# Optimization experiments

Measured on AMD Instinct MI355X. Metric: run time of the kernel, lower is better.

## Reference

```python
import jax, jax.numpy as jnp
import numpy as np

N_NODES = 100000
N_EDGES = 3200000
NFEAT = 256
NCLASS = 64


def setup_inputs() -> dict:
    key = jax.random.key(0)
    k1, k2, k3 = jax.random.split(key, 3)
    x = jax.random.normal(k1, (N_NODES, NFEAT), dtype=jnp.float32)
    W = jax.random.normal(k2, (NFEAT, NCLASS), dtype=jnp.float32) * (1.0 / np.sqrt(NFEAT))
    b = jnp.zeros((NCLASS,), dtype=jnp.float32)
    edge_index = jax.random.randint(k3, (2, N_EDGES), 0, N_NODES, dtype=jnp.int64)
    return {"x": x, "W": W, "b": b, "edge_index": edge_index}


def reference(x, W, b, edge_index):
    # GCNConv (PyG defaults): add self-loops, symmetric D^-1/2 A D^-1/2 norm,
    # linear transform, bias.
    n = x.shape[0]
    loops = jnp.arange(n, dtype=edge_index.dtype)
    src = jnp.concatenate([edge_index[0], loops])  # [E+N]
    dst = jnp.concatenate([edge_index[1], loops])
    ew = jnp.ones(src.shape[0], dtype=x.dtype)
    deg = jax.ops.segment_sum(ew, dst, num_segments=n)  # in-degree incl. self-loop
    dinv = jnp.where(deg > 0, jax.lax.rsqrt(deg), 0.0)
    norm = dinv[src] * dinv[dst]  # [E+N]
    xw = x @ W  # [N, nclass] -- transform before aggregation (small out dim)
    msg = xw[src] * norm[:, None]  # gather + scale
    out = jax.ops.segment_sum(msg, dst, num_segments=n)  # scatter-add
    return out + b
```

## Files before the change

kernel.cpp:

```cpp
#include <hip/hip_runtime.h>
#include <hip/hip_fp16.h>

#define NF 256
#define NC 64
#define BINSZ 256
#define CAP 8832
#define EPB 8192
#define KC 64
#define SCAN_CHUNK 1024


__device__ inline float2 unpack_h2(unsigned int u) {
    __half2 h;
    *reinterpret_cast<unsigned int*>(&h) = u;
    return __half22float2(h);
}
__device__ inline unsigned int pack_h2(float a, float b) {
    __half2 h = __floats2half2_rn(a, b);
    return *reinterpret_cast<unsigned int*>(&h);
}

__global__ __launch_bounds__(256) void k_zcur(int* __restrict__ cursor, int nbin) {
    int i = blockIdx.x * blockDim.x + threadIdx.x;
    if (i < nbin) cursor[i] = 0;
}

__global__ __launch_bounds__(1024) void k_bin3(const int* __restrict__ src,
                                               const int* __restrict__ dst,
                                               int* __restrict__ cursor,
                                               int* __restrict__ binned,
                                               int ne, int nbin) {
    extern __shared__ int lds[];
    int* lcnt = lds;
    int* spk  = lds + nbin;
    unsigned short* sbin = (unsigned short*)(spk + EPB);

    int t = threadIdx.x;
    for (int i = t; i < nbin; i += 1024) lcnt[i] = 0;
    __syncthreads();

    int base = blockIdx.x * EPB;
    int lim = ne - base; if (lim > EPB) lim = EPB;

    for (int k = t; k < lim; k += 1024) {
        int d = dst[base + k];
        int s = src[base + k];
        int bin = d >> 8;
        atomicAdd(&lcnt[bin], 1);
        spk[k]  = (s << 8) | (d & 255);
        sbin[k] = (unsigned short)bin;
    }
    __syncthreads();

    for (int i = t; i < nbin; i += 1024) {
        int c = lcnt[i];
        lcnt[i] = (c > 0) ? atomicAdd(&cursor[i], c) : 0;
    }
    __syncthreads();

    for (int k = t; k < lim; k += 1024) {
        int bin = sbin[k];
        int pos = atomicAdd(&lcnt[bin], 1);
        if (pos < CAP) binned[(long)bin * CAP + pos] = spk[k];
    }
}

__global__ __launch_bounds__(1024) void k_binsort(const int* __restrict__ cursor,
                                                  int* __restrict__ binned,
                                                  int* __restrict__ counts,
                                                  int* __restrict__ rowstart,
                                                  int n) {
    __shared__ int sarr[CAP];
    __shared__ int hist[BINSZ];
    __shared__ int lcur[BINSZ];
    __shared__ int stmp[256];
    int bin = blockIdx.x;
    int t = threadIdx.x;
    if (t < BINSZ) hist[t] = 0;
    __syncthreads();

    int m = cursor[bin]; if (m > CAP) m = CAP;
    int* seg = binned + (long)bin * CAP;

    for (int k = t; k < m; k += 1024) {
        int e = seg[k];
        sarr[k] = e;
        atomicAdd(&hist[e & 255], 1);
    }
    __syncthreads();

    int v = (t < 256) ? hist[t] : 0;
    if (t < 256) stmp[t] = v;
    __syncthreads();
#pragma unroll
    for (int off = 1; off < 256; off <<= 1) {
        int u = (t < 256 && t >= off) ? stmp[t - off] : 0;
        __syncthreads();
        if (t < 256) stmp[t] += u;
        __syncthreads();
    }
    if (t < 256) {
        int excl = stmp[t] - v;
        lcur[t] = excl;
        int node = bin * BINSZ + t;
        if (node < n) {
            counts[node]   = v;
            rowstart[node] = bin * CAP + excl;
        }
    }
    __syncthreads();

    for (int k = t; k < m; k += 1024) {
        int e = sarr[k];
        int pos = atomicAdd(&lcur[e & 255], 1);
        seg[pos] = e >> 8;
    }
}

__global__ __launch_bounds__(256) void k_xw2h(const float* __restrict__ x,
                                              const float* __restrict__ W,
                                              const int* __restrict__ counts,
                                              unsigned int* __restrict__ xwsh, int n) {
    __shared__ float xs[KC][64];
    int t = threadIdx.x;
    int r  = t & 63;
    int cg = __builtin_amdgcn_readfirstlane(t >> 6);
    int rowbase = blockIdx.x * 64;
    int row = rowbase + r;

    float acc[16];
#pragma unroll
    for (int i = 0; i < 16; ++i) acc[i] = 0.0f;

    const float* wp = W + cg * 16;

    int srow = t >> 2, kq = t & 3;
    const float* xg = x + (size_t)(rowbase + srow) * NF;
    bool sv = (rowbase + srow) < n;

    for (int k0 = 0; k0 < NF; k0 += KC) {
        __syncthreads();
#pragma unroll
        for (int j = 0; j < 4; ++j) {
            int kk = kq * 4 + j * 16;
            float4 v;
            if (sv) v = *reinterpret_cast<const float4*>(xg + k0 + kk);
            else    { v.x = v.y = v.z = v.w = 0.0f; }
            xs[kk + 0][srow] = v.x;
            xs[kk + 1][srow] = v.y;
            xs[kk + 2][srow] = v.z;
            xs[kk + 3][srow] = v.w;
        }
        __syncthreads();
#pragma unroll 8
        for (int k = 0; k < KC; ++k) {
            float xv = xs[k][r];
            const float* wk = wp + (size_t)(k0 + k) * NC;
#pragma unroll
            for (int c = 0; c < 16; ++c)
                acc[c] = fmaf(xv, wk[c], acc[c]);
        }
    }

    if (row < n) {
        float di = rsqrtf((float)counts[row] + 1.0f);
        unsigned int buf[8];
#pragma unroll
        for (int i = 0; i < 8; ++i)
            buf[i] = pack_h2(acc[2 * i] * di, acc[2 * i + 1] * di);
        uint4* o = reinterpret_cast<uint4*>(xwsh + (size_t)row * 32 + cg * 8);
        o[0] = make_uint4(buf[0], buf[1], buf[2], buf[3]);
        o[1] = make_uint4(buf[4], buf[5], buf[6], buf[7]);
    }
}

__global__ __launch_bounds__(256) void k_gather_h(const int* __restrict__ rowstart,
                                                  const int* __restrict__ counts,
                                                  const int* __restrict__ csr,
                                                  const unsigned int* __restrict__ xwsh,
                                                  const float* __restrict__ b,
                                                  float* __restrict__ out, int n) {
    int w = (blockIdx.x * blockDim.x + threadIdx.x) >> 6;
    int lane = threadIdx.x & 63;
    if (w >= n) return;
    int half = lane >> 5;
    int lc   = lane & 31;
    int cnt = counts[w];
    int beg = rowstart[w];
    int end = beg + cnt;

    float ax = 0.0f, ay = 0.0f;
    int j = beg;
    for (; j + 8 <= end; j += 8) {
        int s0 = csr[j + 0 + half];
        int s1 = csr[j + 2 + half];
        int s2 = csr[j + 4 + half];
        int s3 = csr[j + 6 + half];
        unsigned int u0 = xwsh[(size_t)s0 * 32 + lc];
        unsigned int u1 = xwsh[(size_t)s1 * 32 + lc];
        unsigned int u2 = xwsh[(size_t)s2 * 32 + lc];
        unsigned int u3 = xwsh[(size_t)s3 * 32 + lc];
        float2 f0 = unpack_h2(u0);
        float2 f1 = unpack_h2(u1);
        float2 f2 = unpack_h2(u2);
        float2 f3 = unpack_h2(u3);
        ax += f0.x; ay += f0.y;
        ax += f1.x; ay += f1.y;
        ax += f2.x; ay += f2.y;
        ax += f3.x; ay += f3.y;
    }
    for (; j < end; j += 2) {
        int jj = j + half;
        unsigned int u = 0;
        if (jj < end) u = xwsh[(size_t)csr[jj] * 32 + lc];
        float2 f = unpack_h2(u);
        ax += f.x; ay += f.y;
    }
    ax += __shfl_xor(ax, 32);
    ay += __shfl_xor(ay, 32);
    float2 sv = unpack_h2(xwsh[(size_t)w * 32 + lc]);
    ax += sv.x; ay += sv.y;

    float di = rsqrtf((float)cnt + 1.0f);
    if (half == 0) {
        float2 o;
        o.x = ax * di + b[2 * lc + 0];
        o.y = ay * di + b[2 * lc + 1];
        *reinterpret_cast<float2*>(out + (size_t)w * NC + 2 * lc) = o;
    }
}


__global__ __launch_bounds__(256) void k_zero(int* __restrict__ p, int n) {
    int i = blockIdx.x * blockDim.x + threadIdx.x;
    if (i < n) p[i] = 0;
}

__global__ __launch_bounds__(256) void k_count(const int* __restrict__ dst,
                                               int* __restrict__ counts, int ne) {
    int e = blockIdx.x * blockDim.x + threadIdx.x;
    if (e < ne) atomicAdd(&counts[dst[e]], 1);
}

__global__ __launch_bounds__(256) void k_scan1(const int* __restrict__ counts,
                                               int* __restrict__ excl,
                                               int* __restrict__ bsum, int n) {
    __shared__ int s[256];
    int t = threadIdx.x;
    int base = blockIdx.x * SCAN_CHUNK + t * 4;
    int v[4];
    int sum = 0;
#pragma unroll
    for (int k = 0; k < 4; ++k) {
        int idx = base + k;
        v[k] = (idx < n) ? counts[idx] : 0;
        sum += v[k];
    }
    s[t] = sum;
    __syncthreads();
#pragma unroll
    for (int off = 1; off < 256; off <<= 1) {
        int xv = (t >= off) ? s[t - off] : 0;
        __syncthreads();
        s[t] += xv;
        __syncthreads();
    }
    int excl_t = s[t] - sum;
    if (t == 255) bsum[blockIdx.x] = s[t];
    int run = excl_t;
#pragma unroll
    for (int k = 0; k < 4; ++k) {
        int idx = base + k;
        if (idx < n) { excl[idx] = run; run += v[k]; }
    }
}

__global__ void k_scan2(int* __restrict__ bsum, int nblk) {
    if (threadIdx.x == 0 && blockIdx.x == 0) {
        int run = 0;
        for (int i = 0; i < nblk; ++i) { int t = bsum[i]; bsum[i] = run; run += t; }
    }
}

__global__ __launch_bounds__(256) void k_scan3(int* __restrict__ rowptr,
                                               const int* __restrict__ bsum, int n) {
    int i = blockIdx.x * blockDim.x + threadIdx.x;
    if (i < n) rowptr[i] += bsum[i / SCAN_CHUNK];
}

__global__ __launch_bounds__(256) void k_fill(const int* __restrict__ src,
                                              const int* __restrict__ dst,
                                              int* __restrict__ rowptr,
                                              int* __restrict__ csr, int ne) {
    int e = blockIdx.x * blockDim.x + threadIdx.x;
    if (e < ne) {
        int pos = atomicAdd(&rowptr[dst[e]], 1);
        csr[pos] = src[e];
    }
}

__global__ __launch_bounds__(256) void k_xw(const float* __restrict__ x,
                                            const float* __restrict__ W,
                                            const int* __restrict__ counts,
                                            float* __restrict__ xws, int n) {
    int r = blockIdx.x * blockDim.x + threadIdx.x;
    if (r >= n) return;
    float acc[NC];
#pragma unroll
    for (int c = 0; c < NC; ++c) acc[c] = 0.0f;
    const float4* xr = reinterpret_cast<const float4*>(x + (size_t)r * NF);
#pragma unroll 1
    for (int k4 = 0; k4 < NF / 4; ++k4) {
        float4 xv = xr[k4];
        const float* wk = W + (size_t)(k4 * 4) * NC;
#pragma unroll
        for (int c = 0; c < NC; ++c) {
            float a = acc[c];
            a = fmaf(xv.x, wk[0 * NC + c], a);
            a = fmaf(xv.y, wk[1 * NC + c], a);
            a = fmaf(xv.z, wk[2 * NC + c], a);
            a = fmaf(xv.w, wk[3 * NC + c], a);
            acc[c] = a;
        }
    }
    float di = rsqrtf((float)counts[r] + 1.0f);
    float4* xo = reinterpret_cast<float4*>(xws + (size_t)r * NC);
#pragma unroll
    for (int c4 = 0; c4 < NC / 4; ++c4) {
        float4 v;
        v.x = acc[4 * c4 + 0] * di;
        v.y = acc[4 * c4 + 1] * di;
        v.z = acc[4 * c4 + 2] * di;
        v.w = acc[4 * c4 + 3] * di;
        xo[c4] = v;
    }
}

__global__ __launch_bounds__(256) void k_gather(const int* __restrict__ rowend,
                                                const int* __restrict__ counts,
                                                const int* __restrict__ csr,
                                                const float* __restrict__ xws,
                                                const float* __restrict__ b,
                                                float* __restrict__ out, int n) {
    int w = (blockIdx.x * blockDim.x + threadIdx.x) >> 6;
    int lane = threadIdx.x & 63;
    if (w >= n) return;
    int cnt = counts[w];
    int end = rowend[w];
    int beg = end - cnt;

    float acc = xws[(size_t)w * NC + lane];
    int j = beg;
    for (; j + 4 <= end; j += 4) {
        int s0 = csr[j + 0], s1 = csr[j + 1], s2 = csr[j + 2], s3 = csr[j + 3];
        float v0 = xws[(size_t)s0 * NC + lane];
        float v1 = xws[(size_t)s1 * NC + lane];
        float v2 = xws[(size_t)s2 * NC + lane];
        float v3 = xws[(size_t)s3 * NC + lane];
        acc += v0; acc += v1; acc += v2; acc += v3;
    }
    for (; j < end; ++j) acc += xws[(size_t)csr[j] * NC + lane];

    float di = rsqrtf((float)cnt + 1.0f);
    out[(size_t)w * NC + lane] = acc * di + b[lane];
}

extern "C" void kernel_launch(void* const* d_in, const int* in_sizes, int n_in,
                              void* d_out, int out_size, void* d_ws, size_t ws_size,
                              hipStream_t stream) {
    const float* x = (const float*)d_in[0];
    const float* W = (const float*)d_in[1];
    const float* b = (const float*)d_in[2];
    const int*   ei = (const int*)d_in[3];
    float* out = (float*)d_out;

    int n  = in_sizes[0] / NF;
    int ne = in_sizes[3] / 2;
    const int* src = ei;
    const int* dst = ei + ne;

    int nbin = (n + BINSZ - 1) / BINSZ;

    size_t curB  = ((size_t)nbin * 4 + 4095) & ~(size_t)4095;
    size_t binB  = (size_t)nbin * CAP * 4;
    size_t cntB  = ((size_t)n * 4 + 4095) & ~(size_t)4095;
    size_t needP = curB + binB + 2 * cntB + (size_t)n * NC * 2;

    if (ws_size >= needP) {
        char* wsb = (char*)d_ws;
        int*   cursor   = (int*)(wsb);
        int*   binned   = (int*)(wsb + curB);
        int*   counts   = (int*)(wsb + curB + binB);
        int*   rowstart = (int*)(wsb + curB + binB + cntB);
        unsigned int* xwsh = (unsigned int*)(wsb + curB + binB + 2 * cntB);

        size_t ldsBin = (size_t)nbin * 4 + (size_t)EPB * 4 + (size_t)EPB * 2;
        k_zcur    <<<(nbin + 255) / 256, 256, 0, stream>>>(cursor, nbin);
        k_bin3    <<<(ne + EPB - 1) / EPB, 1024, ldsBin, stream>>>(src, dst, cursor, binned, ne, nbin);
        k_binsort <<<nbin, 1024, 0, stream>>>(cursor, binned, counts, rowstart, n);
        k_xw2h    <<<(n + 63) / 64, 256, 0, stream>>>(x, W, counts, xwsh, n);
        k_gather_h<<<((size_t)n * 64 + 255) / 256, 256, 0, stream>>>(rowstart, counts, binned, xwsh, b, out, n);
        return;
    }

    size_t cntB2  = (size_t)n * 4;
    size_t bsumB  = 4096;
    size_t csrOff = 2 * cntB2 + bsumB;
    size_t xwsOff = csrOff + (size_t)ne * 4;
    char* wsb = (char*)d_ws;
    int*   counts = (int*)(wsb);
    int*   rowptr = (int*)(wsb + cntB2);
    int*   bsum   = (int*)(wsb + 2 * cntB2);
    int*   csr    = (int*)(wsb + csrOff);
    float* xws    = (float*)(wsb + xwsOff);
    int nblk = (n + SCAN_CHUNK - 1) / SCAN_CHUNK;

    k_zero  <<<(n + 255) / 256, 256, 0, stream>>>(counts, n);
    k_count <<<(ne + 255) / 256, 256, 0, stream>>>(dst, counts, ne);
    k_scan1 <<<nblk, 256, 0, stream>>>(counts, rowptr, bsum, n);
    k_scan2 <<<1, 64, 0, stream>>>(bsum, nblk);
    k_scan3 <<<(n + 255) / 256, 256, 0, stream>>>(rowptr, bsum, n);
    k_xw    <<<(n + 255) / 256, 256, 0, stream>>>(x, W, counts, xws, n);
    k_fill  <<<(ne + 255) / 256, 256, 0, stream>>>(src, dst, rowptr, csr, ne);
    k_gather<<<((size_t)n * 64 + 255) / 256, 256, 0, stream>>>(rowptr, counts, csr, xws, b, out, n);
}
```

Before: 178.9 us.

## Compute x@W with bf16 MFMA plus runtime layout probe and fallback

Replaces the FP32 FMA-based x@W kernel with one that converts x and a pre-transposed W to bf16 and uses 16x16x32 bf16 MFMA instructions, staging output through LDS before writing scaled fp16 rows. A one-wave probe kernel detects the MFMA output layout at runtime, a sampling check kernel compares 256 rows against an FP32 reference, and the old FP32 kernel reruns as a fallback when the check fails. This aims to cut matmul compute time but adds three small launches and lowers input precision to bf16.

```diff
diff --git a/kernel.cpp b/kernel.cpp
--- a/kernel.cpp
+++ b/kernel.cpp
@@ -9,6 +9,9 @@
 #define KC 64
 #define SCAN_CHUNK 1024
 
+typedef __attribute__((ext_vector_type(8))) short bf16x8;
+typedef __attribute__((ext_vector_type(4))) float f32x4;
+
 
 __device__ inline float2 unpack_h2(unsigned int u) {
     __half2 h;
@@ -19,10 +22,51 @@
     __half2 h = __floats2half2_rn(a, b);
     return *reinterpret_cast<unsigned int*>(&h);
 }
-
-__global__ __launch_bounds__(256) void k_zcur(int* __restrict__ cursor, int nbin) {
-    int i = blockIdx.x * blockDim.x + threadIdx.x;
-    if (i < nbin) cursor[i] = 0;
+__device__ inline unsigned short bf16_rne(float f) {
+    unsigned int u = __float_as_uint(f);
+    return (unsigned short)((u + 0x7FFFu + ((u >> 16) & 1u)) >> 16);
+}
+__device__ inline unsigned int pack_bf16x2(float a, float b) {
+    return (unsigned int)bf16_rne(a) | ((unsigned int)bf16_rne(b) << 16);
+}
+
+__global__ __launch_bounds__(256) void k_prep(const float* __restrict__ W,
+                                              unsigned short* __restrict__ Wt,
+                                              int* __restrict__ cursor, int nbin) {
+    int t = blockIdx.x * 256 + threadIdx.x;
+    if (t < 64 * 256) {
+        int col = t >> 8, k = t & 255;
+        Wt[t] = bf16_rne(W[k * 64 + col]);
+    }
+    if (t < nbin) cursor[t] = 0;
+}
+
+__global__ __launch_bounds__(64) void k_probe(int* __restrict__ flag) {
+    int l = threadIdx.x;
+    int fi = l & 15, g = l >> 4;
+    bf16x8 a, b;
+#pragma unroll
+    for (int i = 0; i < 8; ++i) {
+        int k = 8 * g + i;
+        float av = (k == 0) ? (float)(fi + 1) : ((k == 9) ? 1.0f : 0.0f);
+        float bv = (k == 0) ? (float)(fi + 2) : ((k == 9) ? 64.0f : 0.0f);
+        a[i] = (short)bf16_rne(av);
+        b[i] = (short)bf16_rne(bv);
+    }
+    f32x4 d = (f32x4){0.f, 0.f, 0.f, 0.f};
+    d = __builtin_amdgcn_mfma_f32_16x16x32_bf16(a, b, d, 0, 0, 0);
+    int okd = 1, okt = 1;
+#pragma unroll
+    for (int i = 0; i < 4; ++i) {
+        int r = 4 * g + i, c = fi;
+        float expD = (float)((r + 1) * (c + 2) + 64);
+        float expT = (float)((c + 1) * (r + 2) + 64);
+        okd &= (d[i] == expD);
+        okt &= (d[i] == expT);
+    }
+    int alld = __all(okd);
+    int allt = __all(okt);
+    if (l == 0) *flag = alld ? 0 : (allt ? 1 : 2);
 }
 
 __global__ __launch_bounds__(1024) void k_bin3(const int* __restrict__ src,
@@ -117,10 +161,121 @@
     }
 }
 
-__global__ __launch_bounds__(256) void k_xw2h(const float* __restrict__ x,
+__global__ __launch_bounds__(256) void k_xwm(const float* __restrict__ x,
+                                             const unsigned short* __restrict__ Wt,
+                                             const int* __restrict__ counts,
+                                             const int* __restrict__ flag,
+                                             unsigned int* __restrict__ xwsh, int n) {
+    if (flag[0] >= 2) return;
+    int fl = flag[0];
+
+    __shared__ __align__(16) char smem[64 * 66 * 4];
+    unsigned short* xs = (unsigned short*)smem;
+    float* os = (float*)smem;
+
+    int t = threadIdx.x;
+    int rowbase = blockIdx.x * 64;
+    int wv = t >> 6;
+    int l = t & 63;
+
+    int srow = t >> 2;
+    int koff = (t & 3) * 8;
+    const float* xg = x + (size_t)(rowbase + srow) * NF;
+    bool sv = (rowbase + srow) < n;
+
+    f32x4 acc[4];
+#pragma unroll
+    for (int c = 0; c < 4; ++c) acc[c] = (f32x4){0.f, 0.f, 0.f, 0.f};
+
+    int arow = wv * 16 + (l & 15);
+    int aks  = (l >> 4) * 8;
+    const unsigned short* wtl = Wt + (size_t)(l & 15) * 256 + aks;
+
+    for (int k0 = 0; k0 < NF; k0 += 32) {
+        __syncthreads();
+        uint2 w0, w1;
+        if (sv) {
+            float4 f0 = *reinterpret_cast<const float4*>(xg + k0 + koff);
+            float4 f1 = *reinterpret_cast<const float4*>(xg + k0 + koff + 4);
+            w0.x = pack_bf16x2(f0.x, f0.y); w0.y = pack_bf16x2(f0.z, f0.w);
+            w1.x = pack_bf16x2(f1.x, f1.y); w1.y = pack_bf16x2(f1.z, f1.w);
+        } else {
+            w0.x = w0.y = w1.x = w1.y = 0u;
+        }
+        *reinterpret_cast<uint2*>(xs + srow * 40 + koff)     = w0;
+        *reinterpret_cast<uint2*>(xs + srow * 40 + koff + 4) = w1;
+        __syncthreads();
+
+        bf16x8 a = *reinterpret_cast<const bf16x8*>(xs + arow * 40 + aks);
+        const unsigned short* wk = wtl + k0;
+#pragma unroll
+        for (int c = 0; c < 4; ++c) {
+            bf16x8 bfr = *reinterpret_cast<const bf16x8*>(wk + (size_t)c * 16 * 256);
+            acc[c] = __builtin_amdgcn_mfma_f32_16x16x32_bf16(a, bfr, acc[c], 0, 0, 0);
+        }
+    }
+
+    __syncthreads();
+    if (fl == 0) {
+        int r0 = wv * 16 + (l >> 4) * 4;
+        int cn = l & 15;
+#pragma unroll
+        for (int c = 0; c < 4; ++c)
+#pragma unroll
+            for (int i = 0; i < 4; ++i)
+                os[(r0 + i) * 66 + c * 16 + cn] = acc[c][i];
+    } else {
+        int rr = wv * 16 + (l & 15);
+        int c0 = (l >> 4) * 4;
+#pragma unroll
+        for (int c = 0; c < 4; ++c)
+#pragma unroll
+            for (int i = 0; i < 4; ++i)
+                os[rr * 66 + c * 16 + c0 + i] = acc[c][i];
+    }
+    __syncthreads();
+    {
+        int row = t >> 2, cb = t & 3;
+        int grow = rowbase + row;
+        if (grow < n) {
+            float di = rsqrtf((float)counts[grow] + 1.0f);
+            unsigned int buf[8];
+#pragma unroll
+            for (int i2 = 0; i2 < 8; ++i2) {
+                float a0 = os[row * 66 + cb * 16 + 2 * i2 + 0] * di;
+                float a1 = os[row * 66 + cb * 16 + 2 * i2 + 1] * di;
+                buf[i2] = pack_h2(a0, a1);
+            }
+            uint4* o = reinterpret_cast<uint4*>(xwsh + (size_t)grow * 32 + cb * 8);
+            o[0] = make_uint4(buf[0], buf[1], buf[2], buf[3]);
+            o[1] = make_uint4(buf[4], buf[5], buf[6], buf[7]);
+        }
+    }
+}
+
+__global__ __launch_bounds__(64) void k_check(const float* __restrict__ x,
                                               const float* __restrict__ W,
                                               const int* __restrict__ counts,
-                                              unsigned int* __restrict__ xwsh, int n) {
+                                              const unsigned int* __restrict__ xwsh,
+                                              int* __restrict__ flag, int n) {
+    int row = (blockIdx.x * 391) % n;
+    int c = threadIdx.x;
+    float acc = 0.f;
+    for (int k = 0; k < NF; ++k)
+        acc = fmaf(x[(size_t)row * NF + k], W[(size_t)k * NC + c], acc);
+    float ref = acc * rsqrtf((float)counts[row] + 1.0f);
+    unsigned int u = xwsh[(size_t)row * 32 + (c >> 1)];
+    float2 f = unpack_h2(u);
+    float got = (c & 1) ? f.y : f.x;
+    if (fabsf(got - ref) > 0.04f) atomicExch(flag, 2);
+}
+
+__global__ __launch_bounds__(256) void k_xwfix(const float* __restrict__ x,
+                                               const float* __restrict__ W,
+                                               const int* __restrict__ counts,
+                                               const int* __restrict__ flag,
+                                               unsigned int* __restrict__ xwsh, int n) {
+    if (flag[0] < 2) return;
     __shared__ float xs[KC][64];
     int t = threadIdx.x;
     int r  = t & 63;
@@ -384,7 +539,9 @@
     size_t curB  = ((size_t)nbin * 4 + 4095) & ~(size_t)4095;
     size_t binB  = (size_t)nbin * CAP * 4;
     size_t cntB  = ((size_t)n * 4 + 4095) & ~(size_t)4095;
-    size_t needP = curB + binB + 2 * cntB + (size_t)n * NC * 2;
+    size_t xwshB = (size_t)n * NC * 2;
+    size_t WtB   = 65536;
+    size_t needP = curB + binB + 2 * cntB + xwshB + WtB + 4096;
 
     if (ws_size >= needP) {
         char* wsb = (char*)d_ws;
@@ -392,13 +549,18 @@
         int*   binned   = (int*)(wsb + curB);
         int*   counts   = (int*)(wsb + curB + binB);
         int*   rowstart = (int*)(wsb + curB + binB + cntB);
-        unsigned int* xwsh = (unsigned int*)(wsb + curB + binB + 2 * cntB);
+        unsigned int*   xwsh = (unsigned int*)(wsb + curB + binB + 2 * cntB);
+        unsigned short* Wt   = (unsigned short*)(wsb + curB + binB + 2 * cntB + xwshB);
+        int*   flag          = (int*)(wsb + curB + binB + 2 * cntB + xwshB + WtB);
 
         size_t ldsBin = (size_t)nbin * 4 + (size_t)EPB * 4 + (size_t)EPB * 2;
-        k_zcur    <<<(nbin + 255) / 256, 256, 0, stream>>>(cursor, nbin);
+        k_prep    <<<64, 256, 0, stream>>>(W, Wt, cursor, nbin);
+        k_probe   <<<1, 64, 0, stream>>>(flag);
         k_bin3    <<<(ne + EPB - 1) / EPB, 1024, ldsBin, stream>>>(src, dst, cursor, binned, ne, nbin);
         k_binsort <<<nbin, 1024, 0, stream>>>(cursor, binned, counts, rowstart, n);
-        k_xw2h    <<<(n + 63) / 64, 256, 0, stream>>>(x, W, counts, xwsh, n);
+        k_xwm     <<<(n + 63) / 64, 256, 0, stream>>>(x, Wt, counts, flag, xwsh, n);
+        k_check   <<<256, 64, 0, stream>>>(x, W, counts, xwsh, flag, n);
+        k_xwfix   <<<(n + 63) / 64, 256, 0, stream>>>(x, W, counts, flag, xwsh, n);
         k_gather_h<<<((size_t)n * 64 + 255) / 256, 256, 0, stream>>>(rowstart, counts, binned, xwsh, b, out, n);
         return;
     }
```

Result: slower. 228.9 us (+27.9%).
